# Kernel optimization log

Hardware: AMD Instinct MI355X
Metric: run time of the kernel (lower is better)

## Reference

```python
import jax, jax.numpy as jnp
import numpy as np

E = 23  # unique experts
K = 3   # activated experts per token


def setup_inputs() -> dict:
    key = jax.random.key(0)
    ks = jax.random.split(key, 8)
    B, S, D, H = 4, 1024, 1024, 768
    sd = 1.0 / np.sqrt(D)
    sh = 1.0 / np.sqrt(H)
    return {
        "x": jax.random.normal(ks[0], (B, S, D), jnp.float32),
        "gate_W": jax.random.normal(ks[1], (D, E), jnp.float32) * sd,
        "gate_b": jnp.zeros((E,), jnp.float32),
        "route_bias": jnp.zeros((E,), jnp.float32),  # registered buffer 'bias'
        "W1": jax.random.normal(ks[2], (E, D, H), jnp.float32) * sd,
        "b1": jnp.zeros((E, H), jnp.float32),
        "W2": jax.random.normal(ks[3], (E, H, D), jnp.float32) * sh,
        "b2": jnp.zeros((E, D), jnp.float32),
        "sW1": jax.random.normal(ks[4], (D, H), jnp.float32) * sd,
        "sb1": jnp.zeros((H,), jnp.float32),
        "sW2": jax.random.normal(ks[5], (H, D), jnp.float32) * sh,
        "sb2": jnp.zeros((D,), jnp.float32),
    }


def _gelu(x):
    return jax.nn.gelu(x, approximate=False)  # torch nn.GELU default = exact erf


def reference(x, gate_W, gate_b, route_bias, W1, b1, W2, b2, sW1, sb1, sW2, sb2):
    o_shape = x.shape
    xt = x.reshape(-1, o_shape[-1])                       # [N, D]
    N = xt.shape[0]
    gate_weights = jax.nn.sigmoid(xt @ gate_W + gate_b)   # [N, E]
    _, top_idx = jax.lax.top_k(gate_weights + route_bias, K)  # [N, K]
    top_w = jnp.take_along_axis(gate_weights, top_idx, axis=-1)
    top_w = top_w / top_w.sum(axis=-1, keepdims=True)     # [N, K]
    onehot = jax.nn.one_hot(top_idx, E, dtype=xt.dtype)   # [N, K, E]
    combine = jnp.einsum('nke,nk->ne', onehot, top_w)     # [N, E] routed weights
    counts = onehot.sum(axis=(0, 1))                      # tokens per expert
    # dense-equivalent grouped expert MLPs (same math as gather/split/concat)
    h = _gelu(jnp.einsum('nd,edh->enh', xt, W1) + b1[:, None, :])   # [E, N, H]
    y = jnp.einsum('enh,ehd->end', h, W2) + b2[:, None, :]          # [E, N, D]
    routed = jnp.einsum('end,ne->nd', y, combine)
    shared = _gelu(xt @ sW1 + sb1) @ sW2 + sb2
    out = shared + routed
    # aux load-balance loss
    gw_norm = gate_weights / gate_weights.sum(axis=-1, keepdims=True)
    P = gw_norm.mean(axis=0)
    Fvec = (E * counts) / (K * N)
    aux_loss = (P * Fvec).sum()
    return out.reshape(o_shape), aux_loss
```

## Files before the change

### kernel.cpp

```cpp
#include <hip/hip_runtime.h>
#include <hip/hip_bf16.h>
#include <stdint.h>

#define N_TOK 4096
#define DDIM  1024
#define HDIM  768
#define NEXP  23
#define TOPK  3
#define MAXTILE 152
#define SLOTS   19456

typedef float floatx4 __attribute__((ext_vector_type(4)));
typedef short short8  __attribute__((ext_vector_type(8)));

__device__ __forceinline__ short f2bf(float f) {
    __hip_bfloat16 h = __float2bfloat16(f);
    return *reinterpret_cast<short*>(&h);
}
__device__ __forceinline__ float bf2f(short s) {
    unsigned u = ((unsigned)(unsigned short)s) << 16;
    return __uint_as_float(u);
}
__device__ __forceinline__ float gelu_erf(float v) {
    return 0.5f * v * (1.0f + erff(v * 0.70710678118654752f));
}
__device__ __forceinline__ void gl_lds16(const short* g, short* l) {
    __builtin_amdgcn_global_load_lds(
        (const __attribute__((address_space(1))) void*)g,
        (__attribute__((address_space(3))) void*)l, 16, 0, 0);
}

__global__ __launch_bounds__(256) void prep_gate_kernel(
    const float* __restrict__ x, const float* __restrict__ gate_W,
    const float* __restrict__ gate_b, const float* __restrict__ route_bias,
    int* __restrict__ top_idx, float* __restrict__ top_w,
    float* __restrict__ psum_part, short* __restrict__ xb,
    const float* __restrict__ b1, const float* __restrict__ sb1,
    const float* __restrict__ b2, const float* __restrict__ sb2,
    float* __restrict__ bias1_all, float* __restrict__ bias2_all)
{
    const int b = blockIdx.x;
    if (b >= 1024) {
        const int bb = b - 1024;
        if (bb < N_TOK) {
            size_t i = (size_t)bb * 256 + threadIdx.x;
            float4 v = ((const float4*)x)[i];
            short4 o;
            o.x = f2bf(v.x); o.y = f2bf(v.y); o.z = f2bf(v.z); o.w = f2bf(v.w);
            ((short4*)xb)[i] = o;
        } else {
            int i = (bb - N_TOK) * 256 + threadIdx.x;
            if (i < 24 * HDIM) {
                bias1_all[i] = (i < NEXP * HDIM) ? b1[i] : sb1[i - NEXP * HDIM];
            } else {
                int j = i - 24 * HDIM;
                if (j < 24 * DDIM)
                    bias2_all[j] = (j < NEXP * DDIM) ? b2[j] : sb2[j - NEXP * DDIM];
            }
        }
        return;
    }
    const int wave = threadIdx.x >> 6, lane = threadIdx.x & 63;
    const int n = b * 4 + wave;

    __shared__ float gw[64][25];
    float acc[NEXP];
#pragma unroll
    for (int e = 0; e < NEXP; e++) acc[e] = 0.f;

    const float* xr = x + (size_t)n * DDIM;
    for (int c0 = 0; c0 < DDIM; c0 += 64) {
        for (int idx = threadIdx.x; idx < 64 * NEXP; idx += 256)
            gw[idx / NEXP][idx % NEXP] = gate_W[(size_t)c0 * NEXP + idx];
        __syncthreads();
        float xd = xr[c0 + lane];
#pragma unroll
        for (int e = 0; e < NEXP; e++) acc[e] += xd * gw[lane][e];
        __syncthreads();
    }
    for (int off = 32; off > 0; off >>= 1) {
#pragma unroll
        for (int e = 0; e < NEXP; e++) acc[e] += __shfl_xor(acc[e], off, 64);
    }

    float p[NEXP], s = 0.f;
#pragma unroll
    for (int e = 0; e < NEXP; e++) {
        p[e] = 1.f / (1.f + expf(-(acc[e] + gate_b[e])));
        s += p[e];
    }
    const float inv = 1.f / s;

    __shared__ float ps[4][NEXP];
    if (lane == 0) {
#pragma unroll
        for (int e = 0; e < NEXP; e++) ps[wave][e] = p[e] * inv;
        int idx[TOPK]; float w[TOPK]; bool used[NEXP] = {};
        for (int k = 0; k < TOPK; k++) {
            float best = -1e30f; int bi = 0;
            for (int e = 0; e < NEXP; e++) {
                if (!used[e]) {
                    float sc = p[e] + route_bias[e];
                    if (sc > best) { best = sc; bi = e; }
                }
            }
            used[bi] = true; idx[k] = bi; w[k] = p[bi];
        }
        float wsum = w[0] + w[1] + w[2];
        for (int k = 0; k < TOPK; k++) {
            top_idx[n * TOPK + k] = idx[k];
            top_w[n * TOPK + k]   = w[k] / wsum;
        }
    }
    __syncthreads();
    if (threadIdx.x < NEXP) {
        int e = threadIdx.x;
        psum_part[(size_t)b * NEXP + e] =
            ps[0][e] + ps[1][e] + ps[2][e] + ps[3][e];
    }
}

__global__ __launch_bounds__(256) void plan_kernel(
    const int* __restrict__ top_idx, const float* __restrict__ psum_part,
    int* __restrict__ poff, int* __restrict__ cursor, int* __restrict__ tile_e,
    int* __restrict__ Ptot, float* __restrict__ out_aux)
{
    __shared__ int   cnt[NEXP];
    __shared__ float psum[NEXP];
    __shared__ int   tbase[NEXP + 1];
    const int t = threadIdx.x;
    if (t < NEXP) { cnt[t] = 0; psum[t] = 0.f; }
    __syncthreads();

    for (int i = t; i < N_TOK * TOPK; i += 256)
        atomicAdd(&cnt[top_idx[i]], 1);

    float loc[NEXP];
#pragma unroll
    for (int e = 0; e < NEXP; e++) loc[e] = 0.f;
    for (int b = t; b < N_TOK / 4; b += 256) {
        const float* row = psum_part + (size_t)b * NEXP;
#pragma unroll
        for (int e = 0; e < NEXP; e++) loc[e] += row[e];
    }
#pragma unroll
    for (int e = 0; e < NEXP; e++) atomicAdd(&psum[e], loc[e]);
    __syncthreads();

    if (t == 0) {
        int tb = 0; float aux = 0.f;
        for (int e = 0; e < NEXP; e++) {
            tbase[e] = tb;
            float P = psum[e] / (float)N_TOK;
            float F = (float)NEXP * (float)cnt[e] / ((float)TOPK * (float)N_TOK);
            aux += P * F;
            tb += (cnt[e] + 127) >> 7;
        }
        tbase[NEXP] = tb;
        *Ptot = tb << 7;
        *out_aux = aux;
    }
    __syncthreads();
    const int tr = tbase[NEXP];
    if (t < NEXP) { poff[t] = tbase[t] << 7; cursor[t] = 0; }
    for (int i = t; i < MAXTILE; i += 256) {
        int v = -1;
        if (i < tr) {
            for (int e = 0; e < NEXP; e++)
                if (i >= tbase[e] && i < tbase[e + 1]) v = e;
        } else if (i < tr + N_TOK / 128) v = NEXP;
        tile_e[i] = v;
    }
}

__global__ __launch_bounds__(256) void scatter_kernel(
    const int* __restrict__ top_idx, const int* __restrict__ poff,
    int* __restrict__ cursor, int* __restrict__ tok_of_slot,
    int* __restrict__ slot_of_tok, const int* __restrict__ Ptot)
{
    int n = blockIdx.x * 256 + threadIdx.x;
    for (int k = 0; k < TOPK; k++) {
        int e = top_idx[n * TOPK + k];
        int pos = atomicAdd(&cursor[e], 1);
        int slot = poff[e] + pos;
        tok_of_slot[slot] = n;
        slot_of_tok[n * 4 + k] = slot;
    }
    int P = *Ptot;
    tok_of_slot[P + n] = n;
    slot_of_tok[n * 4 + 3] = P + n;
}

__global__ __launch_bounds__(256) void tcvt_kernel(
    const float* __restrict__ W1, const float* __restrict__ sW1, short* __restrict__ W1T,
    const float* __restrict__ W2, const float* __restrict__ sW2, short* __restrict__ W2T)
{
    __shared__ short tile[64][72];
    const int z = blockIdx.z;
    int R, C; const float* s; short* d;
    if (z < 24) {
        R = DDIM; C = HDIM;
        s = (z < NEXP) ? W1 + (size_t)z * DDIM * HDIM : sW1;
        d = W1T + (size_t)z * DDIM * HDIM;
    } else {
        const int e = z - 24;
        R = HDIM; C = DDIM;
        s = (e < NEXP) ? W2 + (size_t)e * HDIM * DDIM : sW2;
        d = W2T + (size_t)e * HDIM * DDIM;
    }
    const int c0 = blockIdx.x * 64, r0 = blockIdx.y * 64;
    if (c0 >= C || r0 >= R) return;
    const int t = threadIdx.x;

    const int rr = t >> 4, cc = (t & 15) << 2;
#pragma unroll
    for (int i = 0; i < 64; i += 16) {
        float4 v = *(const float4*)&s[(size_t)(r0 + i + rr) * C + c0 + cc];
        tile[cc + 0][i + rr] = f2bf(v.x);
        tile[cc + 1][i + rr] = f2bf(v.y);
        tile[cc + 2][i + rr] = f2bf(v.z);
        tile[cc + 3][i + rr] = f2bf(v.w);
    }
    __syncthreads();
    const int cc2 = t >> 3, rr2 = (t & 7) << 3;
#pragma unroll
    for (int j = 0; j < 64; j += 32) {
        *(short8*)&d[(size_t)(c0 + j + cc2) * R + r0 + rr2] =
            *(const short8*)&tile[j + cc2][rr2];
    }
}

template <bool FFN1>
__global__ __launch_bounds__(256) void gemm_kernel(
    const short* __restrict__ Abase, const int* __restrict__ tok_of_slot,
    const int* __restrict__ tile_e, const short* __restrict__ Wall,
    const float* __restrict__ bias_all, short* __restrict__ outb)
{
    constexpr int KD = FFN1 ? DDIM : HDIM;
    constexpr int NC = FFN1 ? HDIM : DDIM;
    constexpr int KI = KD / 32;

    const int tile = blockIdx.y;
    const int e = tile_e[tile];
    if (e < 0) return;
    const int slot0 = tile * 128;
    const int n0 = blockIdx.x * 128;

    __shared__ short As[3][128 * 32];
    __shared__ short Bs[3][128 * 32];

    const int t = threadIdx.x;
    const int w = t >> 6, l = t & 63;
    const int quad = l >> 4, l16 = l & 15;
    const int wr = w >> 1, wc = w & 1;

    const int ra0 = w * 32 + (l >> 2);
    const int ra1 = ra0 + 16;
    const int ko  = (l & 3) << 3;

    const short *ap0, *ap1;
    if constexpr (FFN1) {
        int t0 = tok_of_slot[slot0 + ra0];
        int t1 = tok_of_slot[slot0 + ra1];
        t0 = ((unsigned)t0 < (unsigned)N_TOK) ? t0 : 0;
        t1 = ((unsigned)t1 < (unsigned)N_TOK) ? t1 : 0;
        ap0 = Abase + (size_t)t0 * KD + ko;
        ap1 = Abase + (size_t)t1 * KD + ko;
    } else {
        ap0 = Abase + (size_t)(slot0 + ra0) * KD + ko;
        ap1 = Abase + (size_t)(slot0 + ra1) * KD + ko;
    }
    const short* bbase = Wall + (size_t)e * NC * KD + (size_t)n0 * KD;
    const short* bp0 = bbase + (size_t)ra0 * KD + ko;
    const short* bp1 = bbase + (size_t)ra1 * KD + ko;

    const int ldo0 = (w * 32) * 32;
    const int ldo1 = (w * 32 + 16) * 32;

    floatx4 acc[4][4] = {};

#pragma unroll
    for (int p = 0; p < 3; p++) {
        gl_lds16(ap0, &As[p][ldo0]); gl_lds16(ap1, &As[p][ldo1]);
        gl_lds16(bp0, &Bs[p][ldo0]); gl_lds16(bp1, &Bs[p][ldo1]);
        ap0 += 32; ap1 += 32; bp0 += 32; bp1 += 32;
    }

#pragma unroll
    for (int k = 0; k < KI; k++) {
        if (k < KI - 2)       asm volatile("s_waitcnt vmcnt(8)" ::: "memory");
        else if (k == KI - 2) asm volatile("s_waitcnt vmcnt(4)" ::: "memory");
        else                  asm volatile("s_waitcnt vmcnt(0)" ::: "memory");
        asm volatile("s_barrier" ::: "memory");

        const int s = k % 3;
        short8 af[4], bf[4];
#pragma unroll
        for (int i = 0; i < 4; i++)
            af[i] = *(const short8*)&As[s][(wr * 64 + i * 16 + l16) * 32 + quad * 8];
#pragma unroll
        for (int j = 0; j < 4; j++)
            bf[j] = *(const short8*)&Bs[s][(wc * 64 + j * 16 + l16) * 32 + quad * 8];
#pragma unroll
        for (int i = 0; i < 4; i++)
#pragma unroll
            for (int j = 0; j < 4; j++)
                acc[i][j] = __builtin_amdgcn_mfma_f32_16x16x32_bf16(af[i], bf[j], acc[i][j], 0, 0, 0);

        asm volatile("s_waitcnt lgkmcnt(0)" ::: "memory");
        asm volatile("s_barrier" ::: "memory");
        if (k + 3 < KI) {
            gl_lds16(ap0, &As[s][ldo0]); gl_lds16(ap1, &As[s][ldo1]);
            gl_lds16(bp0, &Bs[s][ldo0]); gl_lds16(bp1, &Bs[s][ldo1]);
            ap0 += 32; ap1 += 32; bp0 += 32; bp1 += 32;
        }
    }

    const int bias_off = e * NC;
#pragma unroll
    for (int j = 0; j < 4; j++) {
        const int col = n0 + wc * 64 + j * 16 + l16;
        const float bv = bias_all[bias_off + col];
#pragma unroll
        for (int i = 0; i < 4; i++)
#pragma unroll
            for (int r = 0; r < 4; r++) {
                const int row = slot0 + wr * 64 + i * 16 + quad * 4 + r;
                float v = acc[i][j][r] + bv;
                outb[(size_t)row * NC + col] = f2bf(FFN1 ? gelu_erf(v) : v);
            }
    }
}

__global__ __launch_bounds__(256) void combine_kernel(
    const short* __restrict__ ybuf, const int* __restrict__ slot_of_tok,
    const float* __restrict__ top_w, float* __restrict__ out)
{
    const int n = blockIdx.x;
    const int c = threadIdx.x;
    const int s0 = slot_of_tok[n * 4 + 0];
    const int s1 = slot_of_tok[n * 4 + 1];
    const int s2 = slot_of_tok[n * 4 + 2];
    const int ss = slot_of_tok[n * 4 + 3];
    const float w0 = top_w[n * 3 + 0];
    const float w1 = top_w[n * 3 + 1];
    const float w2 = top_w[n * 3 + 2];

    short4 y0 = ((const short4*)(ybuf + (size_t)s0 * DDIM))[c];
    short4 y1 = ((const short4*)(ybuf + (size_t)s1 * DDIM))[c];
    short4 y2 = ((const short4*)(ybuf + (size_t)s2 * DDIM))[c];
    short4 ys = ((const short4*)(ybuf + (size_t)ss * DDIM))[c];

    float4 o;
    o.x = bf2f(ys.x) + w0 * bf2f(y0.x) + w1 * bf2f(y1.x) + w2 * bf2f(y2.x);
    o.y = bf2f(ys.y) + w0 * bf2f(y0.y) + w1 * bf2f(y1.y) + w2 * bf2f(y2.y);
    o.z = bf2f(ys.z) + w0 * bf2f(y0.z) + w1 * bf2f(y1.z) + w2 * bf2f(y2.z);
    o.w = bf2f(ys.w) + w0 * bf2f(y0.w) + w1 * bf2f(y1.w) + w2 * bf2f(y2.w);
    ((float4*)(out + (size_t)n * DDIM))[c] = o;
}

extern "C" void kernel_launch(void* const* d_in, const int* in_sizes, int n_in,
                              void* d_out, int out_size, void* d_ws, size_t ws_size,
                              hipStream_t stream)
{
    const float* x          = (const float*)d_in[0];
    const float* gate_W     = (const float*)d_in[1];
    const float* gate_b     = (const float*)d_in[2];
    const float* route_bias = (const float*)d_in[3];
    const float* W1         = (const float*)d_in[4];
    const float* b1         = (const float*)d_in[5];
    const float* W2         = (const float*)d_in[6];
    const float* b2         = (const float*)d_in[7];
    const float* sW1        = (const float*)d_in[8];
    const float* sb1        = (const float*)d_in[9];
    const float* sW2        = (const float*)d_in[10];
    const float* sb2        = (const float*)d_in[11];
    float* out = (float*)d_out;

    uint8_t* ws = (uint8_t*)d_ws;
    int*   top_idx   = (int*)(ws);
    float* top_w     = (float*)(ws + 49152);
    int*   poff      = (int*)(ws + 98304);
    int*   cursor    = (int*)(ws + 98432);
    int*   Ptot      = (int*)(ws + 98560);
    int*   tile_e    = (int*)(ws + 98688);
    float* psum_part = (float*)(ws + 99328);
    int*   tok_slot  = (int*)(ws + 193536);
    int*   slot_tok  = (int*)(ws + 271360);
    float* bias1_all = (float*)(ws + 336896);
    float* bias2_all = (float*)(ws + 410624);
    short* xb        = (short*)(ws + 512000);
    short* W1T       = (short*)(ws + 8902656);
    short* W2T       = (short*)(ws + 46651392);
    short* hbuf      = (short*)(ws + 84400128);
    short* ybuf      = (short*)(ws + 512000);

    prep_gate_kernel<<<1024 + N_TOK + (24 * (HDIM + DDIM)) / 256, 256, 0, stream>>>(
        x, gate_W, gate_b, route_bias, top_idx, top_w, psum_part,
        xb, b1, sb1, b2, sb2, bias1_all, bias2_all);
    tcvt_kernel<<<dim3(16, 16, 48), 256, 0, stream>>>(W1, sW1, W1T, W2, sW2, W2T);
    plan_kernel<<<1, 256, 0, stream>>>(top_idx, psum_part, poff, cursor, tile_e,
                                       Ptot, out + (size_t)N_TOK * DDIM);
    scatter_kernel<<<N_TOK / 256, 256, 0, stream>>>(top_idx, poff, cursor,
                                                    tok_slot, slot_tok, Ptot);

    gemm_kernel<true><<<dim3(HDIM / 128, MAXTILE), 256, 0, stream>>>(
        xb, tok_slot, tile_e, W1T, bias1_all, hbuf);
    gemm_kernel<false><<<dim3(DDIM / 128, MAXTILE), 256, 0, stream>>>(
        hbuf, tok_slot, tile_e, W2T, bias2_all, ybuf);
    combine_kernel<<<N_TOK, 256, 0, stream>>>(ybuf, slot_tok, top_w, out);
}
```

Before: 482.7 us.

## Fuse weight transpose into prep, merge scatter into plan, remap GEMM blocks

Folds the weight transpose/convert kernel into the prep kernel and the scatter kernel into the single-block plan kernel, which cuts two launches and lets the transpose overlap with gating. The GEMM now remaps block IDs so that consecutive tiles land on the same XCD, for better L2 reuse. Its epilogue stages the output through swizzled LDS so each row is written with 16-byte coalesced stores. The trade-off is that scatter now runs serially in one block, 12K slot writes handled by 256 threads.

```diff
diff --git a/kernel.cpp b/kernel.cpp
--- a/kernel.cpp
+++ b/kernel.cpp
@@ -30,26 +30,35 @@
         (__attribute__((address_space(3))) void*)l, 16, 0, 0);
 }
 
-__global__ __launch_bounds__(256) void prep_gate_kernel(
+#define PREP_GATE   1024
+#define PREP_XCVT   N_TOK
+#define PREP_BIAS   168
+#define PREP_TCVT   9216
+#define PREP_GRID   (PREP_GATE + PREP_XCVT + PREP_BIAS + PREP_TCVT)
+
+__global__ __launch_bounds__(256) void prep_kernel(
     const float* __restrict__ x, const float* __restrict__ gate_W,
     const float* __restrict__ gate_b, const float* __restrict__ route_bias,
     int* __restrict__ top_idx, float* __restrict__ top_w,
     float* __restrict__ psum_part, short* __restrict__ xb,
     const float* __restrict__ b1, const float* __restrict__ sb1,
     const float* __restrict__ b2, const float* __restrict__ sb2,
-    float* __restrict__ bias1_all, float* __restrict__ bias2_all)
+    float* __restrict__ bias1_all, float* __restrict__ bias2_all,
+    const float* __restrict__ W1, const float* __restrict__ sW1, short* __restrict__ W1T,
+    const float* __restrict__ W2, const float* __restrict__ sW2, short* __restrict__ W2T)
 {
+    __shared__ float ldsbuf[2304];
     const int b = blockIdx.x;
-    if (b >= 1024) {
-        const int bb = b - 1024;
-        if (bb < N_TOK) {
+    if (b >= PREP_GATE) {
+        const int bb = b - PREP_GATE;
+        if (bb < PREP_XCVT) {
             size_t i = (size_t)bb * 256 + threadIdx.x;
             float4 v = ((const float4*)x)[i];
             short4 o;
             o.x = f2bf(v.x); o.y = f2bf(v.y); o.z = f2bf(v.z); o.w = f2bf(v.w);
             ((short4*)xb)[i] = o;
-        } else {
-            int i = (bb - N_TOK) * 256 + threadIdx.x;
+        } else if (bb < PREP_XCVT + PREP_BIAS) {
+            int i = (bb - PREP_XCVT) * 256 + threadIdx.x;
             if (i < 24 * HDIM) {
                 bias1_all[i] = (i < NEXP * HDIM) ? b1[i] : sb1[i - NEXP * HDIM];
             } else {
@@ -57,13 +66,50 @@
                 if (j < 24 * DDIM)
                     bias2_all[j] = (j < NEXP * DDIM) ? b2[j] : sb2[j - NEXP * DDIM];
             }
+        } else {
+            int idx = bb - (PREP_XCVT + PREP_BIAS);
+            const float* s; short* d; int R, C, cx, cy;
+            if (idx < 24 * 192) {
+                const int w = idx / 192, rem = idx % 192;
+                R = DDIM; C = HDIM; cx = rem % 12; cy = rem / 12;
+                s = (w < NEXP) ? W1 + (size_t)w * DDIM * HDIM : sW1;
+                d = W1T + (size_t)w * DDIM * HDIM;
+            } else {
+                idx -= 24 * 192;
+                const int w = idx / 192, rem = idx % 192;
+                R = HDIM; C = DDIM; cx = rem % 16; cy = rem / 16;
+                s = (w < NEXP) ? W2 + (size_t)w * HDIM * DDIM : sW2;
+                d = W2T + (size_t)w * HDIM * DDIM;
+            }
+            const int c0 = cx * 64, r0 = cy * 64;
+            const int t = threadIdx.x;
+            short (*tile)[72] = (short(*)[72])ldsbuf;
+
+            const int rr = t >> 4, cc = (t & 15) << 2;
+#pragma unroll
+            for (int i = 0; i < 64; i += 16) {
+                float4 v = *(const float4*)&s[(size_t)(r0 + i + rr) * C + c0 + cc];
+                tile[cc + 0][i + rr] = f2bf(v.x);
+                tile[cc + 1][i + rr] = f2bf(v.y);
+                tile[cc + 2][i + rr] = f2bf(v.z);
+                tile[cc + 3][i + rr] = f2bf(v.w);
+            }
+            __syncthreads();
+            const int cc2 = t >> 3, rr2 = (t & 7) << 3;
+#pragma unroll
+            for (int j = 0; j < 64; j += 32) {
+                *(short8*)&d[(size_t)(c0 + j + cc2) * R + r0 + rr2] =
+                    *(const short8*)&tile[j + cc2][rr2];
+            }
         }
         return;
     }
     const int wave = threadIdx.x >> 6, lane = threadIdx.x & 63;
     const int n = b * 4 + wave;
 
-    __shared__ float gw[64][25];
+    float (*gw)[25]  = (float(*)[25])ldsbuf;
+    float (*ps)[NEXP] = (float(*)[NEXP])(ldsbuf + 1600);
+
     float acc[NEXP];
 #pragma unroll
     for (int e = 0; e < NEXP; e++) acc[e] = 0.f;
@@ -91,7 +137,6 @@
     }
     const float inv = 1.f / s;
 
-    __shared__ float ps[4][NEXP];
     if (lane == 0) {
 #pragma unroll
         for (int e = 0; e < NEXP; e++) ps[wave][e] = p[e] * inv;
@@ -122,14 +167,15 @@
 
 __global__ __launch_bounds__(256) void plan_kernel(
     const int* __restrict__ top_idx, const float* __restrict__ psum_part,
-    int* __restrict__ poff, int* __restrict__ cursor, int* __restrict__ tile_e,
-    int* __restrict__ Ptot, float* __restrict__ out_aux)
+    int* __restrict__ tile_e, int* __restrict__ tok_of_slot,
+    int* __restrict__ slot_of_tok, float* __restrict__ out_aux)
 {
     __shared__ int   cnt[NEXP];
     __shared__ float psum[NEXP];
     __shared__ int   tbase[NEXP + 1];
+    __shared__ int   lcur[NEXP];
     const int t = threadIdx.x;
-    if (t < NEXP) { cnt[t] = 0; psum[t] = 0.f; }
+    if (t < NEXP) { cnt[t] = 0; psum[t] = 0.f; lcur[t] = 0; }
     __syncthreads();
 
     for (int i = t; i < N_TOK * TOPK; i += 256)
@@ -157,12 +203,11 @@
             tb += (cnt[e] + 127) >> 7;
         }
         tbase[NEXP] = tb;
-        *Ptot = tb << 7;
         *out_aux = aux;
     }
     __syncthreads();
     const int tr = tbase[NEXP];
-    if (t < NEXP) { poff[t] = tbase[t] << 7; cursor[t] = 0; }
+    const int P  = tr << 7;
     for (int i = t; i < MAXTILE; i += 256) {
         int v = -1;
         if (i < tr) {
@@ -171,62 +216,17 @@
         } else if (i < tr + N_TOK / 128) v = NEXP;
         tile_e[i] = v;
     }
-}
-
-__global__ __launch_bounds__(256) void scatter_kernel(
-    const int* __restrict__ top_idx, const int* __restrict__ poff,
-    int* __restrict__ cursor, int* __restrict__ tok_of_slot,
-    int* __restrict__ slot_of_tok, const int* __restrict__ Ptot)
-{
-    int n = blockIdx.x * 256 + threadIdx.x;
-    for (int k = 0; k < TOPK; k++) {
-        int e = top_idx[n * TOPK + k];
-        int pos = atomicAdd(&cursor[e], 1);
-        int slot = poff[e] + pos;
+    for (int i = t; i < N_TOK * TOPK; i += 256) {
+        const int e = top_idx[i];
+        const int pos = atomicAdd(&lcur[e], 1);
+        const int slot = (tbase[e] << 7) + pos;
+        const int n = i / 3, k = i - n * 3;
         tok_of_slot[slot] = n;
         slot_of_tok[n * 4 + k] = slot;
     }
-    int P = *Ptot;
-    tok_of_slot[P + n] = n;
-    slot_of_tok[n * 4 + 3] = P + n;
-}
-
-__global__ __launch_bounds__(256) void tcvt_kernel(
-    const float* __restrict__ W1, const float* __restrict__ sW1, short* __restrict__ W1T,
-    const float* __restrict__ W2, const float* __restrict__ sW2, short* __restrict__ W2T)
-{
-    __shared__ short tile[64][72];
-    const int z = blockIdx.z;
-    int R, C; const float* s; short* d;
-    if (z < 24) {
-        R = DDIM; C = HDIM;
-        s = (z < NEXP) ? W1 + (size_t)z * DDIM * HDIM : sW1;
-        d = W1T + (size_t)z * DDIM * HDIM;
-    } else {
-        const int e = z - 24;
-        R = HDIM; C = DDIM;
-        s = (e < NEXP) ? W2 + (size_t)e * HDIM * DDIM : sW2;
-        d = W2T + (size_t)e * HDIM * DDIM;
-    }
-    const int c0 = blockIdx.x * 64, r0 = blockIdx.y * 64;
-    if (c0 >= C || r0 >= R) return;
-    const int t = threadIdx.x;
-
-    const int rr = t >> 4, cc = (t & 15) << 2;
-#pragma unroll
-    for (int i = 0; i < 64; i += 16) {
-        float4 v = *(const float4*)&s[(size_t)(r0 + i + rr) * C + c0 + cc];
-        tile[cc + 0][i + rr] = f2bf(v.x);
-        tile[cc + 1][i + rr] = f2bf(v.y);
-        tile[cc + 2][i + rr] = f2bf(v.z);
-        tile[cc + 3][i + rr] = f2bf(v.w);
-    }
-    __syncthreads();
-    const int cc2 = t >> 3, rr2 = (t & 7) << 3;
-#pragma unroll
-    for (int j = 0; j < 64; j += 32) {
-        *(short8*)&d[(size_t)(c0 + j + cc2) * R + r0 + rr2] =
-            *(const short8*)&tile[j + cc2][rr2];
+    for (int n = t; n < N_TOK; n += 256) {
+        tok_of_slot[P + n] = n;
+        slot_of_tok[n * 4 + 3] = P + n;
     }
 }
 
@@ -239,15 +239,25 @@
     constexpr int KD = FFN1 ? DDIM : HDIM;
     constexpr int NC = FFN1 ? HDIM : DDIM;
     constexpr int KI = KD / 32;
-
-    const int tile = blockIdx.y;
+    constexpr int GX = NC / 128;
+    constexpr int NWG = GX * MAXTILE;
+    constexpr int Q = NWG / 8, RM = NWG % 8;
+
+    int bid = blockIdx.y * GX + blockIdx.x;
+    {
+        const int xcd = bid & 7, off = bid >> 3;
+        bid = (xcd < RM) ? (xcd * (Q + 1) + off)
+                         : (RM * (Q + 1) + (xcd - RM) * Q + off);
+    }
+    const int tile = bid / GX;
     const int e = tile_e[tile];
     if (e < 0) return;
     const int slot0 = tile * 128;
-    const int n0 = blockIdx.x * 128;
-
-    __shared__ short As[3][128 * 32];
-    __shared__ short Bs[3][128 * 32];
+    const int n0 = (bid - tile * GX) * 128;
+
+    __shared__ short smem[3 * 4096 * 2];
+    short* const As = smem;
+    short* const Bs = smem + 3 * 4096;
 
     const int t = threadIdx.x;
     const int w = t >> 6, l = t & 63;
@@ -281,8 +291,8 @@
 
 #pragma unroll
     for (int p = 0; p < 3; p++) {
-        gl_lds16(ap0, &As[p][ldo0]); gl_lds16(ap1, &As[p][ldo1]);
-        gl_lds16(bp0, &Bs[p][ldo0]); gl_lds16(bp1, &Bs[p][ldo1]);
+        gl_lds16(ap0, As + p * 4096 + ldo0); gl_lds16(ap1, As + p * 4096 + ldo1);
+        gl_lds16(bp0, Bs + p * 4096 + ldo0); gl_lds16(bp1, Bs + p * 4096 + ldo1);
         ap0 += 32; ap1 += 32; bp0 += 32; bp1 += 32;
     }
 
@@ -297,10 +307,10 @@
         short8 af[4], bf[4];
 #pragma unroll
         for (int i = 0; i < 4; i++)
-            af[i] = *(const short8*)&As[s][(wr * 64 + i * 16 + l16) * 32 + quad * 8];
+            af[i] = *(const short8*)(As + s * 4096 + (wr * 64 + i * 16 + l16) * 32 + quad * 8);
 #pragma unroll
         for (int j = 0; j < 4; j++)
-            bf[j] = *(const short8*)&Bs[s][(wc * 64 + j * 16 + l16) * 32 + quad * 8];
+            bf[j] = *(const short8*)(Bs + s * 4096 + (wc * 64 + j * 16 + l16) * 32 + quad * 8);
 #pragma unroll
         for (int i = 0; i < 4; i++)
 #pragma unroll
@@ -310,25 +320,36 @@
         asm volatile("s_waitcnt lgkmcnt(0)" ::: "memory");
         asm volatile("s_barrier" ::: "memory");
         if (k + 3 < KI) {
-            gl_lds16(ap0, &As[s][ldo0]); gl_lds16(ap1, &As[s][ldo1]);
-            gl_lds16(bp0, &Bs[s][ldo0]); gl_lds16(bp1, &Bs[s][ldo1]);
+            gl_lds16(ap0, As + s * 4096 + ldo0); gl_lds16(ap1, As + s * 4096 + ldo1);
+            gl_lds16(bp0, Bs + s * 4096 + ldo0); gl_lds16(bp1, Bs + s * 4096 + ldo1);
             ap0 += 32; ap1 += 32; bp0 += 32; bp1 += 32;
         }
     }
 
-    const int bias_off = e * NC;
+    short* const OT = smem;
+    const int bias_off = e * NC + n0;
 #pragma unroll
     for (int j = 0; j < 4; j++) {
-        const int col = n0 + wc * 64 + j * 16 + l16;
-        const float bv = bias_all[bias_off + col];
+        const int colL = wc * 64 + j * 16 + l16;
+        const float bv = bias_all[bias_off + colL];
+        const int cg = colL >> 3, wi = colL & 7;
 #pragma unroll
         for (int i = 0; i < 4; i++)
 #pragma unroll
             for (int r = 0; r < 4; r++) {
-                const int row = slot0 + wr * 64 + i * 16 + quad * 4 + r;
+                const int rowL = wr * 64 + i * 16 + quad * 4 + r;
                 float v = acc[i][j][r] + bv;
-                outb[(size_t)row * NC + col] = f2bf(FFN1 ? gelu_erf(v) : v);
-            }
+                if constexpr (FFN1) v = gelu_erf(v);
+                OT[rowL * 128 + (((cg ^ ((rowL >> 2) & 3)) << 3) | wi)] = f2bf(v);
+            }
+    }
+    __syncthreads();
+#pragma unroll
+    for (int p = 0; p < 8; p++) {
+        const int rowL = p * 16 + (t >> 4);
+        const int g = t & 15;
+        const short8 v = *(const short8*)(OT + rowL * 128 + ((g ^ ((rowL >> 2) & 3)) << 3));
+        *(short8*)&outb[(size_t)(slot0 + rowL) * NC + n0 + g * 8] = v;
     }
 }
 
@@ -380,9 +401,6 @@
     uint8_t* ws = (uint8_t*)d_ws;
     int*   top_idx   = (int*)(ws);
     float* top_w     = (float*)(ws + 49152);
-    int*   poff      = (int*)(ws + 98304);
-    int*   cursor    = (int*)(ws + 98432);
-    int*   Ptot      = (int*)(ws + 98560);
     int*   tile_e    = (int*)(ws + 98688);
     float* psum_part = (float*)(ws + 99328);
     int*   tok_slot  = (int*)(ws + 193536);
@@ -395,14 +413,13 @@
     short* hbuf      = (short*)(ws + 84400128);
     short* ybuf      = (short*)(ws + 512000);
 
-    prep_gate_kernel<<<1024 + N_TOK + (24 * (HDIM + DDIM)) / 256, 256, 0, stream>>>(
+    prep_kernel<<<PREP_GRID, 256, 0, stream>>>(
         x, gate_W, gate_b, route_bias, top_idx, top_w, psum_part,
-        xb, b1, sb1, b2, sb2, bias1_all, bias2_all);
-    tcvt_kernel<<<dim3(16, 16, 48), 256, 0, stream>>>(W1, sW1, W1T, W2, sW2, W2T);
-    plan_kernel<<<1, 256, 0, stream>>>(top_idx, psum_part, poff, cursor, tile_e,
-                                       Ptot, out + (size_t)N_TOK * DDIM);
-    scatter_kernel<<<N_TOK / 256, 256, 0, stream>>>(top_idx, poff, cursor,
-                                                    tok_slot, slot_tok, Ptot);
+        xb, b1, sb1, b2, sb2, bias1_all, bias2_all,
+        W1, sW1, W1T, W2, sW2, W2T);
+    plan_kernel<<<1, 256, 0, stream>>>(top_idx, psum_part, tile_e,
+                                       tok_slot, slot_tok,
+                                       out + (size_t)N_TOK * DDIM);
 
     gemm_kernel<true><<<dim3(HDIM / 128, MAXTILE), 256, 0, stream>>>(
         xb, tok_slot, tile_e, W1T, bias1_all, hbuf);
```

New measurement: 412.4 us. 1.17x faster.
